# Optimization experiments

Hardware: AMD Instinct MI355X
Metric: run time of the kernel (lower is better)

Reference implementation:

```python
import jax, jax.numpy as jnp
import numpy as np

N, NQ, M, DQ, DK, DV, H = 4, 512, 512, 256, 256, 256, 256


def setup_inputs() -> dict:
    key = jax.random.key(0)
    ks = jax.random.split(key, 6)
    scale_q = 1.0 / np.sqrt(DQ)
    scale_k = 1.0 / np.sqrt(DK)
    scale_v = 1.0 / np.sqrt(H)
    return {
        "query": jax.random.normal(ks[0], (N, NQ, DQ), jnp.float32),
        "key": jax.random.normal(ks[1], (N, M, DK), jnp.float32),
        "value": jax.random.normal(ks[2], (N, M, DV), jnp.float32),
        "W_q": jax.random.normal(ks[3], (DQ, H), jnp.float32) * scale_q,
        "W_k": jax.random.normal(ks[4], (DK, H), jnp.float32) * scale_k,
        "W_v": jax.random.normal(ks[5], (H,), jnp.float32) * scale_v,
    }


def reference(query, key, value, W_q, W_k, W_v):
    # project: (N, n, H) and (N, m, H)
    q = jnp.einsum("bnd,dh->bnh", query, W_q)
    k = jnp.einsum("bmd,dh->bmh", key, W_k)
    # broadcast add -> (N, n, m, H), tanh, project H->1 -> scores (N, n, m)
    scores = jnp.einsum("bnmh,h->bnm", jnp.tanh(q[:, :, None, :] + k[:, None, :, :]), W_v)
    attn = jax.nn.softmax(scores, axis=-1)  # (N, n, m)
    return jnp.einsum("bnm,bmv->bnv", attn, value)
```

## Files before the change

kernel.cpp:

```cpp
#include <hip/hip_runtime.h>
#include <hip/hip_bf16.h>

#define NB 4
#define NQL 512
#define ML 512
#define DDIM 256
#define HDIM 256

static constexpr float TWO_LOG2E = 2.8853900817779268f;
static constexpr float LOG2E     = 1.4426950408889634f;

__global__ __launch_bounds__(256) void proj_kernel(
    const float* __restrict__ q_src, const float* __restrict__ k_src,
    const float* __restrict__ Wq,    const float* __restrict__ Wk,
    float* __restrict__ EqT,         float* __restrict__ EkT)
{
    const int z = blockIdx.z;
    const int b = z & 3;
    const int which = z >> 2;
    const float* __restrict__ src  = which ? k_src : q_src;
    const float* __restrict__ W    = which ? Wk    : Wq;
    float* __restrict__       outT = which ? EkT   : EqT;

    const int l0 = blockIdx.x * 32;
    const int h0 = blockIdx.y * 64;
    const int t  = threadIdx.x;
    const int tx = t & 15;
    const int ty = t >> 4;

    __shared__ __align__(16) float sX[32][36];
    __shared__ __align__(16) float sW[32][68];

    float acc[2][4];
    #pragma unroll
    for (int i = 0; i < 2; i++)
        #pragma unroll
        for (int j = 0; j < 4; j++) acc[i][j] = 0.f;

    const int llA = t >> 3, dgA = t & 7;
    const int ddB = t >> 3, hgB = t & 7;

    for (int d0 = 0; d0 < DDIM; d0 += 32) {
        float4 xv = *(const float4*)&src[(size_t)(b * NQL + l0 + llA) * DDIM + d0 + dgA * 4];
        const float* wrow = &W[(size_t)(d0 + ddB) * HDIM + h0 + hgB * 8];
        float4 wa = ((const float4*)wrow)[0];
        float4 wb = ((const float4*)wrow)[1];
        __syncthreads();
        sX[dgA * 4 + 0][llA] = xv.x;
        sX[dgA * 4 + 1][llA] = xv.y;
        sX[dgA * 4 + 2][llA] = xv.z;
        sX[dgA * 4 + 3][llA] = xv.w;
        *(float4*)&sW[ddB][hgB * 8]     = wa;
        *(float4*)&sW[ddB][hgB * 8 + 4] = wb;
        __syncthreads();
        #pragma unroll
        for (int dd = 0; dd < 32; dd++) {
            float4 w4 = *(const float4*)&sW[dd][tx * 4];
            float2 x2 = *(const float2*)&sX[dd][ty * 2];
            acc[0][0] = fmaf(x2.x, w4.x, acc[0][0]);
            acc[0][1] = fmaf(x2.x, w4.y, acc[0][1]);
            acc[0][2] = fmaf(x2.x, w4.z, acc[0][2]);
            acc[0][3] = fmaf(x2.x, w4.w, acc[0][3]);
            acc[1][0] = fmaf(x2.y, w4.x, acc[1][0]);
            acc[1][1] = fmaf(x2.y, w4.y, acc[1][1]);
            acc[1][2] = fmaf(x2.y, w4.z, acc[1][2]);
            acc[1][3] = fmaf(x2.y, w4.w, acc[1][3]);
        }
    }

    #pragma unroll
    for (int j = 0; j < 4; j++) {
        float2 o;
        o.x = __builtin_amdgcn_exp2f(acc[0][j] * TWO_LOG2E);
        o.y = __builtin_amdgcn_exp2f(acc[1][j] * TWO_LOG2E);
        *(float2*)&outT[(size_t)(b * HDIM + h0 + tx * 4 + j) * NQL + l0 + ty * 2] = o;
    }
}

__global__ __launch_bounds__(256) void scores_kernel(
    const float* __restrict__ EqT, const float* __restrict__ EkT,
    const float* __restrict__ Wv, float* __restrict__ S)
{
    const int b  = blockIdx.z;
    const int m0 = blockIdx.x * 64;
    const int n0 = blockIdx.y * 16;
    const int t  = threadIdx.x;
    const int tx = t & 15;
    const int ty = t >> 4;

    __shared__ __align__(16) float sQ[16][36];
    __shared__ __align__(16) float sK[32][68];
    __shared__ __align__(16) float sWV[32];

    float acc0 = 0.f, acc1 = 0.f, acc2 = 0.f, acc3 = 0.f;
    float swv = 0.f;

    const int hhA = t >> 3;
    const int cgA = t & 7;

    for (int h0 = 0; h0 < HDIM; h0 += 32) {
        float2 qv = *(const float2*)&EqT[(size_t)(b * HDIM + h0 + hhA) * NQL + n0 + cgA * 2];
        const float* krow = &EkT[(size_t)(b * HDIM + h0 + hhA) * ML + m0 + cgA * 8];
        float4 ka = ((const float4*)krow)[0];
        float4 kb = ((const float4*)krow)[1];
        float wv_ld = (t < 32) ? Wv[h0 + t] : 0.f;
        __syncthreads();
        sQ[cgA * 2 + 0][hhA] = qv.x;
        sQ[cgA * 2 + 1][hhA] = qv.y;
        *(float4*)&sK[hhA][cgA * 8]     = ka;
        *(float4*)&sK[hhA][cgA * 8 + 4] = kb;
        if (t < 32) sWV[t] = wv_ld;
        __syncthreads();
        #pragma unroll
        for (int g = 0; g < 8; g++) {
            float4 q4 = *(const float4*)&sQ[ty][g * 4];
            float4 w4 = *(const float4*)&sWV[g * 4];
            float qs[4] = {q4.x, q4.y, q4.z, q4.w};
            float ws[4] = {w4.x, w4.y, w4.z, w4.w};
            #pragma unroll
            for (int j = 0; j < 4; j++) {
                float4 k4 = *(const float4*)&sK[g * 4 + j][tx * 4];
                float wv = ws[j];
                swv += wv;
                const float nw2 = -2.0f * wv;
                float a0 = fmaf(qs[j], k4.x, 1.0f);
                float a1 = fmaf(qs[j], k4.y, 1.0f);
                float a2 = fmaf(qs[j], k4.z, 1.0f);
                float a3 = fmaf(qs[j], k4.w, 1.0f);
                float r01 = __builtin_amdgcn_rcpf(a0 * a1);
                float r23 = __builtin_amdgcn_rcpf(a2 * a3);
                acc0 = fmaf(nw2, r01 * a1, acc0);
                acc1 = fmaf(nw2, r01 * a0, acc1);
                acc2 = fmaf(nw2, r23 * a3, acc2);
                acc3 = fmaf(nw2, r23 * a2, acc3);
            }
        }
    }

    float4 o = {swv + acc0, swv + acc1, swv + acc2, swv + acc3};
    *(float4*)&S[(size_t)(b * NQL + n0 + ty) * ML + m0 + tx * 4] = o;
}

__global__ __launch_bounds__(256) void sav_kernel(
    const float* __restrict__ S, const float* __restrict__ V,
    float* __restrict__ O)
{
    const int b  = blockIdx.z;
    const int v0 = blockIdx.x * 64;
    const int n0 = blockIdx.y * 16;
    const int t  = threadIdx.x;

    __shared__ __align__(16) float sP[16][516];
    __shared__ __align__(16) float sRed[16][16];

    const int row = t >> 4;
    const int seg = t & 15;
    {
        const float* srow = &S[(size_t)(b * NQL + n0 + row) * ML + seg * 32];
        float psum = 0.f;
        #pragma unroll
        for (int i = 0; i < 8; i++) {
            float4 sv = ((const float4*)srow)[i];
            float4 e;
            e.x = __builtin_amdgcn_exp2f(sv.x * LOG2E);
            e.y = __builtin_amdgcn_exp2f(sv.y * LOG2E);
            e.z = __builtin_amdgcn_exp2f(sv.z * LOG2E);
            e.w = __builtin_amdgcn_exp2f(sv.w * LOG2E);
            *(float4*)&sP[row][seg * 32 + i * 4] = e;
            psum += (e.x + e.y) + (e.z + e.w);
        }
        sRed[row][seg] = psum;
    }
    __syncthreads();

    const int tx = t & 15;
    const int ty = t >> 4;
    float rs = 0.f;
    #pragma unroll
    for (int i = 0; i < 16; i++) rs += sRed[tx][i];
    const float inv = 1.0f / rs;

    float4 acc = {0.f, 0.f, 0.f, 0.f};
    const float* vbase = &V[(size_t)b * ML * DDIM + v0 + ty * 4];
    #pragma unroll 2
    for (int m4 = 0; m4 < 128; m4++) {
        float4 a4 = *(const float4*)&sP[tx][m4 * 4];
        float4 va = *(const float4*)&vbase[(size_t)(m4 * 4 + 0) * DDIM];
        float4 vb = *(const float4*)&vbase[(size_t)(m4 * 4 + 1) * DDIM];
        float4 vc = *(const float4*)&vbase[(size_t)(m4 * 4 + 2) * DDIM];
        float4 vd = *(const float4*)&vbase[(size_t)(m4 * 4 + 3) * DDIM];
        acc.x = fmaf(a4.x, va.x, acc.x);
        acc.y = fmaf(a4.x, va.y, acc.y);
        acc.z = fmaf(a4.x, va.z, acc.z);
        acc.w = fmaf(a4.x, va.w, acc.w);
        acc.x = fmaf(a4.y, vb.x, acc.x);
        acc.y = fmaf(a4.y, vb.y, acc.y);
        acc.z = fmaf(a4.y, vb.z, acc.z);
        acc.w = fmaf(a4.y, vb.w, acc.w);
        acc.x = fmaf(a4.z, vc.x, acc.x);
        acc.y = fmaf(a4.z, vc.y, acc.y);
        acc.z = fmaf(a4.z, vc.z, acc.z);
        acc.w = fmaf(a4.z, vc.w, acc.w);
        acc.x = fmaf(a4.w, vd.x, acc.x);
        acc.y = fmaf(a4.w, vd.y, acc.y);
        acc.z = fmaf(a4.w, vd.z, acc.z);
        acc.w = fmaf(a4.w, vd.w, acc.w);
    }

    float4 o;
    o.x = acc.x * inv; o.y = acc.y * inv; o.z = acc.z * inv; o.w = acc.w * inv;
    *(float4*)&O[(size_t)(b * NQL + n0 + tx) * DDIM + v0 + ty * 4] = o;
}

extern "C" void kernel_launch(void* const* d_in, const int* in_sizes, int n_in,
                              void* d_out, int out_size, void* d_ws, size_t ws_size,
                              hipStream_t stream)
{
    const float* query = (const float*)d_in[0];
    const float* key   = (const float*)d_in[1];
    const float* value = (const float*)d_in[2];
    const float* Wq    = (const float*)d_in[3];
    const float* Wk    = (const float*)d_in[4];
    const float* Wv    = (const float*)d_in[5];
    float* out = (float*)d_out;

    float* EqT = (float*)d_ws;
    float* EkT = EqT + (size_t)NB * HDIM * NQL;
    float* S   = EkT + (size_t)NB * HDIM * ML;

    dim3 gProj(NQL / 32, HDIM / 64, NB * 2);
    proj_kernel<<<gProj, 256, 0, stream>>>(query, key, Wq, Wk, EqT, EkT);

    dim3 gSc(ML / 64, NQL / 16, NB);
    scores_kernel<<<gSc, 256, 0, stream>>>(EqT, EkT, Wv, S);

    dim3 gSav(DDIM / 64, NQL / 16, NB);
    sav_kernel<<<gSav, 256, 0, stream>>>(S, value, out);
}
```

Baseline: 145.5 us.

## Split scores over H into four partials with 4x4 register tiles, sum in softmax

The scores kernel now tiles 64x64 (n,m) per block, with each thread computing a 4x4 register tile instead of a 1x4 strip. This raises reuse of the shared Q and K values. The H reduction is split into four 64-wide slices across the grid z dimension, and each slice writes a partial score buffer. The softmax/AV kernel then sums the four partials. The gain is more arithmetic per shared-memory load and enough blocks to fill the device, at the cost of extra workspace and four times the score reads in the last kernel.

After: 157.8 us. +8.5%, slower.

```diff
diff --git a/kernel.cpp b/kernel.cpp
--- a/kernel.cpp
+++ b/kernel.cpp
@@ -6,6 +6,7 @@
 #define ML 512
 #define DDIM 256
 #define HDIM 256
+#define PSZ ((size_t)NB * NQL * ML)
 
 static constexpr float TWO_LOG2E = 2.8853900817779268f;
 static constexpr float LOG2E     = 1.4426950408889634f;
@@ -79,70 +80,92 @@
 
 __global__ __launch_bounds__(256) void scores_kernel(
     const float* __restrict__ EqT, const float* __restrict__ EkT,
-    const float* __restrict__ Wv, float* __restrict__ S)
-{
-    const int b  = blockIdx.z;
+    const float* __restrict__ Wv, float* __restrict__ Sp)
+{
+    const int z  = blockIdx.z;
+    const int b  = z & 3;
+    const int p  = z >> 2;
+    const int h0 = p * 64;
     const int m0 = blockIdx.x * 64;
-    const int n0 = blockIdx.y * 16;
+    const int n0 = blockIdx.y * 64;
     const int t  = threadIdx.x;
     const int tx = t & 15;
     const int ty = t >> 4;
 
-    __shared__ __align__(16) float sQ[16][36];
-    __shared__ __align__(16) float sK[32][68];
-    __shared__ __align__(16) float sWV[32];
-
-    float acc0 = 0.f, acc1 = 0.f, acc2 = 0.f, acc3 = 0.f;
+    __shared__ __align__(16) float sQ[64][68];
+    __shared__ __align__(16) float sK[64][68];
+    __shared__ __align__(16) float sWV[64];
+
+    {
+        const int hh = t >> 2, cg = t & 3;
+        const float* qsrc = &EqT[(size_t)(b * HDIM + h0 + hh) * NQL + n0 + cg * 16];
+        const float* ksrc = &EkT[(size_t)(b * HDIM + h0 + hh) * ML  + m0 + cg * 16];
+        float4 q0 = ((const float4*)qsrc)[0];
+        float4 q1 = ((const float4*)qsrc)[1];
+        float4 q2 = ((const float4*)qsrc)[2];
+        float4 q3 = ((const float4*)qsrc)[3];
+        float4 k0 = ((const float4*)ksrc)[0];
+        float4 k1 = ((const float4*)ksrc)[1];
+        float4 k2 = ((const float4*)ksrc)[2];
+        float4 k3 = ((const float4*)ksrc)[3];
+        *(float4*)&sQ[hh][cg * 16 + 0]  = q0;
+        *(float4*)&sQ[hh][cg * 16 + 4]  = q1;
+        *(float4*)&sQ[hh][cg * 16 + 8]  = q2;
+        *(float4*)&sQ[hh][cg * 16 + 12] = q3;
+        *(float4*)&sK[hh][cg * 16 + 0]  = k0;
+        *(float4*)&sK[hh][cg * 16 + 4]  = k1;
+        *(float4*)&sK[hh][cg * 16 + 8]  = k2;
+        *(float4*)&sK[hh][cg * 16 + 12] = k3;
+        if (t < 64) sWV[t] = Wv[h0 + t];
+    }
+    __syncthreads();
+
+    float acc[4][4];
+    #pragma unroll
+    for (int i = 0; i < 4; i++)
+        #pragma unroll
+        for (int j = 0; j < 4; j++) acc[i][j] = 0.f;
     float swv = 0.f;
 
-    const int hhA = t >> 3;
-    const int cgA = t & 7;
-
-    for (int h0 = 0; h0 < HDIM; h0 += 32) {
-        float2 qv = *(const float2*)&EqT[(size_t)(b * HDIM + h0 + hhA) * NQL + n0 + cgA * 2];
-        const float* krow = &EkT[(size_t)(b * HDIM + h0 + hhA) * ML + m0 + cgA * 8];
-        float4 ka = ((const float4*)krow)[0];
-        float4 kb = ((const float4*)krow)[1];
-        float wv_ld = (t < 32) ? Wv[h0 + t] : 0.f;
-        __syncthreads();
-        sQ[cgA * 2 + 0][hhA] = qv.x;
-        sQ[cgA * 2 + 1][hhA] = qv.y;
-        *(float4*)&sK[hhA][cgA * 8]     = ka;
-        *(float4*)&sK[hhA][cgA * 8 + 4] = kb;
-        if (t < 32) sWV[t] = wv_ld;
-        __syncthreads();
-        #pragma unroll
-        for (int g = 0; g < 8; g++) {
-            float4 q4 = *(const float4*)&sQ[ty][g * 4];
-            float4 w4 = *(const float4*)&sWV[g * 4];
+    for (int h4 = 0; h4 < 16; h4++) {
+        float4 wv4 = *(const float4*)&sWV[h4 * 4];
+        float wvs[4] = {wv4.x, wv4.y, wv4.z, wv4.w};
+        #pragma unroll
+        for (int u = 0; u < 4; u++) {
+            const int hh = h4 * 4 + u;
+            float4 q4 = *(const float4*)&sQ[hh][ty * 4];
+            float4 k4 = *(const float4*)&sK[hh][tx * 4];
+            const float wv  = wvs[u];
+            swv += wv;
+            const float nw2 = -2.0f * wv;
             float qs[4] = {q4.x, q4.y, q4.z, q4.w};
-            float ws[4] = {w4.x, w4.y, w4.z, w4.w};
             #pragma unroll
-            for (int j = 0; j < 4; j++) {
-                float4 k4 = *(const float4*)&sK[g * 4 + j][tx * 4];
-                float wv = ws[j];
-                swv += wv;
-                const float nw2 = -2.0f * wv;
-                float a0 = fmaf(qs[j], k4.x, 1.0f);
-                float a1 = fmaf(qs[j], k4.y, 1.0f);
-                float a2 = fmaf(qs[j], k4.z, 1.0f);
-                float a3 = fmaf(qs[j], k4.w, 1.0f);
+            for (int i = 0; i < 4; i++) {
+                float a0 = fmaf(qs[i], k4.x, 1.0f);
+                float a1 = fmaf(qs[i], k4.y, 1.0f);
+                float a2 = fmaf(qs[i], k4.z, 1.0f);
+                float a3 = fmaf(qs[i], k4.w, 1.0f);
                 float r01 = __builtin_amdgcn_rcpf(a0 * a1);
                 float r23 = __builtin_amdgcn_rcpf(a2 * a3);
-                acc0 = fmaf(nw2, r01 * a1, acc0);
-                acc1 = fmaf(nw2, r01 * a0, acc1);
-                acc2 = fmaf(nw2, r23 * a3, acc2);
-                acc3 = fmaf(nw2, r23 * a2, acc3);
+                acc[i][0] = fmaf(nw2, r01 * a1, acc[i][0]);
+                acc[i][1] = fmaf(nw2, r01 * a0, acc[i][1]);
+                acc[i][2] = fmaf(nw2, r23 * a3, acc[i][2]);
+                acc[i][3] = fmaf(nw2, r23 * a2, acc[i][3]);
             }
         }
     }
 
-    float4 o = {swv + acc0, swv + acc1, swv + acc2, swv + acc3};
-    *(float4*)&S[(size_t)(b * NQL + n0 + ty) * ML + m0 + tx * 4] = o;
+    float* srow = &Sp[p * PSZ + (size_t)(b * NQL + n0 + ty * 4) * ML + m0 + tx * 4];
+    #pragma unroll
+    for (int i = 0; i < 4; i++) {
+        float4 o = {swv + acc[i][0], swv + acc[i][1],
+                    swv + acc[i][2], swv + acc[i][3]};
+        *(float4*)&srow[(size_t)i * ML] = o;
+    }
 }
 
 __global__ __launch_bounds__(256) void sav_kernel(
-    const float* __restrict__ S, const float* __restrict__ V,
+    const float* __restrict__ Sp, const float* __restrict__ V,
     float* __restrict__ O)
 {
     const int b  = blockIdx.z;
@@ -156,11 +179,19 @@
     const int row = t >> 4;
     const int seg = t & 15;
     {
-        const float* srow = &S[(size_t)(b * NQL + n0 + row) * ML + seg * 32];
+        const float* srow = &Sp[(size_t)(b * NQL + n0 + row) * ML + seg * 32];
         float psum = 0.f;
         #pragma unroll
         for (int i = 0; i < 8; i++) {
-            float4 sv = ((const float4*)srow)[i];
+            float4 s0 = ((const float4*)(srow + 0 * PSZ))[i];
+            float4 s1 = ((const float4*)(srow + 1 * PSZ))[i];
+            float4 s2 = ((const float4*)(srow + 2 * PSZ))[i];
+            float4 s3 = ((const float4*)(srow + 3 * PSZ))[i];
+            float4 sv;
+            sv.x = (s0.x + s1.x) + (s2.x + s3.x);
+            sv.y = (s0.y + s1.y) + (s2.y + s3.y);
+            sv.z = (s0.z + s1.z) + (s2.z + s3.z);
+            sv.w = (s0.w + s1.w) + (s2.w + s3.w);
             float4 e;
             e.x = __builtin_amdgcn_exp2f(sv.x * LOG2E);
             e.y = __builtin_amdgcn_exp2f(sv.y * LOG2E);
@@ -226,14 +257,14 @@
 
     float* EqT = (float*)d_ws;
     float* EkT = EqT + (size_t)NB * HDIM * NQL;
-    float* S   = EkT + (size_t)NB * HDIM * ML;
+    float* Sp  = EkT + (size_t)NB * HDIM * ML;
 
     dim3 gProj(NQL / 32, HDIM / 64, NB * 2);
     proj_kernel<<<gProj, 256, 0, stream>>>(query, key, Wq, Wk, EqT, EkT);
 
-    dim3 gSc(ML / 64, NQL / 16, NB);
-    scores_kernel<<<gSc, 256, 0, stream>>>(EqT, EkT, Wv, S);
+    dim3 gSc(ML / 64, NQL / 64, NB * 4);
+    scores_kernel<<<gSc, 256, 0, stream>>>(EqT, EkT, Wv, Sp);
 
     dim3 gSav(DDIM / 64, NQL / 16, NB);
-    sav_kernel<<<gSav, 256, 0, stream>>>(S, value, out);
-}
+    sav_kernel<<<gSav, 256, 0, stream>>>(Sp, value, out);
+}
```

## Compute two query rows per thread with packed float2 math and fuse exp into scores

Applied to the files above, without the earlier changes.

The scores kernel now handles 32 query rows per block, with each thread computing two rows using 2-wide vector types so the compiler can emit packed FP32 multiply/FMA. The Q tile is stored without a transpose via float4 stores, and the K values in shared memory are reused across both rows. The softmax exponential moves from the sav kernel into the scores epilogue, so the redundant exp across the four v-blocks goes away. In exchange there are half as many scores blocks and more registers per thread, which could lower occupancy.

Result: no change. 143.8 us (-1.2%).

```diff
diff --git a/kernel.cpp b/kernel.cpp
--- a/kernel.cpp
+++ b/kernel.cpp
@@ -9,6 +9,8 @@
 
 static constexpr float TWO_LOG2E = 2.8853900817779268f;
 static constexpr float LOG2E     = 1.4426950408889634f;
+
+typedef float v2f __attribute__((ext_vector_type(2)));
 
 __global__ __launch_bounds__(256) void proj_kernel(
     const float* __restrict__ q_src, const float* __restrict__ k_src,
@@ -79,70 +81,85 @@
 
 __global__ __launch_bounds__(256) void scores_kernel(
     const float* __restrict__ EqT, const float* __restrict__ EkT,
-    const float* __restrict__ Wv, float* __restrict__ S)
+    const float* __restrict__ Wv, float* __restrict__ P)
 {
     const int b  = blockIdx.z;
     const int m0 = blockIdx.x * 64;
-    const int n0 = blockIdx.y * 16;
+    const int n0 = blockIdx.y * 32;
     const int t  = threadIdx.x;
     const int tx = t & 15;
     const int ty = t >> 4;
 
-    __shared__ __align__(16) float sQ[16][36];
+    __shared__ __align__(16) float sQ[32][36];
     __shared__ __align__(16) float sK[32][68];
     __shared__ __align__(16) float sWV[32];
 
-    float acc0 = 0.f, acc1 = 0.f, acc2 = 0.f, acc3 = 0.f;
+    v2f acc0 = {0.f, 0.f}, acc1 = {0.f, 0.f};
+    v2f acc2 = {0.f, 0.f}, acc3 = {0.f, 0.f};
     float swv = 0.f;
 
-    const int hhA = t >> 3;
-    const int cgA = t & 7;
+    const int hhA = t >> 3, cgA = t & 7;
 
     for (int h0 = 0; h0 < HDIM; h0 += 32) {
-        float2 qv = *(const float2*)&EqT[(size_t)(b * HDIM + h0 + hhA) * NQL + n0 + cgA * 2];
+        float4 qv = *(const float4*)&EqT[(size_t)(b * HDIM + h0 + hhA) * NQL + n0 + cgA * 4];
         const float* krow = &EkT[(size_t)(b * HDIM + h0 + hhA) * ML + m0 + cgA * 8];
         float4 ka = ((const float4*)krow)[0];
         float4 kb = ((const float4*)krow)[1];
         float wv_ld = (t < 32) ? Wv[h0 + t] : 0.f;
         __syncthreads();
-        sQ[cgA * 2 + 0][hhA] = qv.x;
-        sQ[cgA * 2 + 1][hhA] = qv.y;
+        *(float4*)&sQ[hhA][cgA * 4]     = qv;
         *(float4*)&sK[hhA][cgA * 8]     = ka;
         *(float4*)&sK[hhA][cgA * 8 + 4] = kb;
         if (t < 32) sWV[t] = wv_ld;
         __syncthreads();
         #pragma unroll
-        for (int g = 0; g < 8; g++) {
-            float4 q4 = *(const float4*)&sQ[ty][g * 4];
-            float4 w4 = *(const float4*)&sWV[g * 4];
-            float qs[4] = {q4.x, q4.y, q4.z, q4.w};
-            float ws[4] = {w4.x, w4.y, w4.z, w4.w};
+        for (int h4 = 0; h4 < 8; h4++) {
+            float4 wv4 = *(const float4*)&sWV[h4 * 4];
+            float wvs[4] = {wv4.x, wv4.y, wv4.z, wv4.w};
             #pragma unroll
-            for (int j = 0; j < 4; j++) {
-                float4 k4 = *(const float4*)&sK[g * 4 + j][tx * 4];
-                float wv = ws[j];
+            for (int u = 0; u < 4; u++) {
+                const int hh = h4 * 4 + u;
+                v2f   q2 = *(const v2f*)&sQ[hh][ty * 2];
+                float4 k4 = *(const float4*)&sK[hh][tx * 4];
+                const float wv = wvs[u];
                 swv += wv;
                 const float nw2 = -2.0f * wv;
-                float a0 = fmaf(qs[j], k4.x, 1.0f);
-                float a1 = fmaf(qs[j], k4.y, 1.0f);
-                float a2 = fmaf(qs[j], k4.z, 1.0f);
-                float a3 = fmaf(qs[j], k4.w, 1.0f);
-                float r01 = __builtin_amdgcn_rcpf(a0 * a1);
-                float r23 = __builtin_amdgcn_rcpf(a2 * a3);
-                acc0 = fmaf(nw2, r01 * a1, acc0);
-                acc1 = fmaf(nw2, r01 * a0, acc1);
-                acc2 = fmaf(nw2, r23 * a3, acc2);
-                acc3 = fmaf(nw2, r23 * a2, acc3);
+                v2f a0 = q2 * k4.x + 1.0f;
+                v2f a1 = q2 * k4.y + 1.0f;
+                v2f a2 = q2 * k4.z + 1.0f;
+                v2f a3 = q2 * k4.w + 1.0f;
+                v2f p01 = a0 * a1;
+                v2f p23 = a2 * a3;
+                v2f r01, r23;
+                r01.x = __builtin_amdgcn_rcpf(p01.x);
+                r01.y = __builtin_amdgcn_rcpf(p01.y);
+                r23.x = __builtin_amdgcn_rcpf(p23.x);
+                r23.y = __builtin_amdgcn_rcpf(p23.y);
+                acc0 += (r01 * a1) * nw2;
+                acc1 += (r01 * a0) * nw2;
+                acc2 += (r23 * a3) * nw2;
+                acc3 += (r23 * a2) * nw2;
             }
         }
     }
 
-    float4 o = {swv + acc0, swv + acc1, swv + acc2, swv + acc3};
-    *(float4*)&S[(size_t)(b * NQL + n0 + ty) * ML + m0 + tx * 4] = o;
+    v2f s0 = acc0 + swv, s1 = acc1 + swv, s2 = acc2 + swv, s3 = acc3 + swv;
+    float4 row0, row1;
+    row0.x = __builtin_amdgcn_exp2f(s0.x * LOG2E);
+    row0.y = __builtin_amdgcn_exp2f(s1.x * LOG2E);
+    row0.z = __builtin_amdgcn_exp2f(s2.x * LOG2E);
+    row0.w = __builtin_amdgcn_exp2f(s3.x * LOG2E);
+    row1.x = __builtin_amdgcn_exp2f(s0.y * LOG2E);
+    row1.y = __builtin_amdgcn_exp2f(s1.y * LOG2E);
+    row1.z = __builtin_amdgcn_exp2f(s2.y * LOG2E);
+    row1.w = __builtin_amdgcn_exp2f(s3.y * LOG2E);
+    float* prow = &P[(size_t)(b * NQL + n0 + ty * 2) * ML + m0 + tx * 4];
+    *(float4*)&prow[0]  = row0;
+    *(float4*)&prow[ML] = row1;
 }
 
 __global__ __launch_bounds__(256) void sav_kernel(
-    const float* __restrict__ S, const float* __restrict__ V,
+    const float* __restrict__ P, const float* __restrict__ V,
     float* __restrict__ O)
 {
     const int b  = blockIdx.z;
@@ -156,16 +173,11 @@
     const int row = t >> 4;
     const int seg = t & 15;
     {
-        const float* srow = &S[(size_t)(b * NQL + n0 + row) * ML + seg * 32];
+        const float* prow = &P[(size_t)(b * NQL + n0 + row) * ML + seg * 32];
         float psum = 0.f;
         #pragma unroll
         for (int i = 0; i < 8; i++) {
-            float4 sv = ((const float4*)srow)[i];
-            float4 e;
-            e.x = __builtin_amdgcn_exp2f(sv.x * LOG2E);
-            e.y = __builtin_amdgcn_exp2f(sv.y * LOG2E);
-            e.z = __builtin_amdgcn_exp2f(sv.z * LOG2E);
-            e.w = __builtin_amdgcn_exp2f(sv.w * LOG2E);
+            float4 e = ((const float4*)prow)[i];
             *(float4*)&sP[row][seg * 32 + i * 4] = e;
             psum += (e.x + e.y) + (e.z + e.w);
         }
@@ -226,14 +238,14 @@
 
     float* EqT = (float*)d_ws;
     float* EkT = EqT + (size_t)NB * HDIM * NQL;
-    float* S   = EkT + (size_t)NB * HDIM * ML;
+    float* P   = EkT + (size_t)NB * HDIM * ML;
 
     dim3 gProj(NQL / 32, HDIM / 64, NB * 2);
     proj_kernel<<<gProj, 256, 0, stream>>>(query, key, Wq, Wk, EqT, EkT);
 
-    dim3 gSc(ML / 64, NQL / 16, NB);
-    scores_kernel<<<gSc, 256, 0, stream>>>(EqT, EkT, Wv, S);
+    dim3 gSc(ML / 64, NQL / 32, NB);
+    scores_kernel<<<gSc, 256, 0, stream>>>(EqT, EkT, Wv, P);
 
     dim3 gSav(DDIM / 64, NQL / 16, NB);
-    sav_kernel<<<gSav, 256, 0, stream>>>(S, value, out);
-}
+    sav_kernel<<<gSav, 256, 0, stream>>>(P, value, out);
+}
```
